# Performance work log

Measured on AMD Instinct MI355X. Metric: run time of the kernel, lower is better.

## Reference

```python
import jax, jax.numpy as jnp
import numpy as np

HEADS = 12
HEAD_SIZE = 64
NEG_BIG = 1e12


def _rope_sin_cos(seq_len, head_size, dtype):
    # embeddings[n, 2i] = sin(n * 10000^(-2i/d)), [n, 2i+1] = cos(...)
    pos = jnp.arange(seq_len, dtype=dtype)                      # [s]
    idx = jnp.arange(head_size // 2, dtype=dtype)               # [d/2]
    inv_freq = jnp.power(jnp.asarray(10000.0, dtype), -2.0 * idx / head_size)
    ang = jnp.einsum('n,d->nd', pos, inv_freq)                  # [s, d/2]
    # cos_pos / sin_pos: repeat_interleave each frequency twice -> [1, s, 1, d]
    cos = jnp.repeat(jnp.cos(ang), 2, axis=-1)[None, :, None, :]
    sin = jnp.repeat(jnp.sin(ang), 2, axis=-1)[None, :, None, :]
    return sin, cos


def _rotate_half_interleaved(x):
    # stack([-x[..., 1::2], x[..., ::2]], -1).reshape_as(x)
    x2 = jnp.stack([-x[..., 1::2], x[..., ::2]], axis=-1)
    return x2.reshape(x.shape)


def setup_inputs() -> dict:
    key = jax.random.key(0)
    k1, k2 = jax.random.split(key)
    bs, s, h = 16, 512, 768
    hidden = jax.random.normal(k1, (bs, s, h), dtype=jnp.float32)
    attention_mask = jnp.ones((bs, s), dtype=jnp.int32)
    W = jax.random.normal(k2, (h, HEADS * 2 * HEAD_SIZE), dtype=jnp.float32) * (h ** -0.5)
    b = jnp.zeros((HEADS * 2 * HEAD_SIZE,), dtype=jnp.float32)
    return {"hidden": hidden, "attention_mask": attention_mask, "W": W, "b": b}


def reference(hidden, attention_mask, W, b):
    bs, s, _ = hidden.shape
    x = hidden @ W + b                                           # [b, s, heads*2*hd]
    x = x.reshape(bs, s, HEADS, 2, HEAD_SIZE)
    qw, kw = x[..., 0, :], x[..., 1, :]                          # [b, s, h, d]

    sin, cos = _rope_sin_cos(s, HEAD_SIZE, hidden.dtype)
    qw = qw * cos + _rotate_half_interleaved(qw) * sin
    kw = kw * cos + _rotate_half_interleaved(kw) * sin

    logits = jnp.einsum('bmhd,bnhd->bhmn', qw, kw)               # [b, h, s, s]

    am = attention_mask.astype(logits.dtype)
    pad_mask = 1.0 - am[:, None, None, :] * am[:, None, :, None]
    logits = logits - pad_mask * NEG_BIG

    tril = jnp.tril(jnp.ones((s, s), dtype=logits.dtype), k=-1)  # strictly lower
    logits = logits - tril[None, None, :, :] * NEG_BIG

    return logits / (HEAD_SIZE ** 0.5)
```

## Files before the change

kernel.cpp:

```cpp
#include <hip/hip_runtime.h>
#include <math.h>

#define HEADS 12
#define HSZ   64
#define SEQ   512
#define HID   768
#define NOUT  1536
#define NEGQ  1.25e11f

typedef _Float16 f16x8 __attribute__((ext_vector_type(8)));
typedef _Float16 f16x4 __attribute__((ext_vector_type(4)));
typedef float    f32x4 __attribute__((ext_vector_type(4)));
typedef int      i32x4 __attribute__((ext_vector_type(4)));
typedef int      i32x8 __attribute__((ext_vector_type(8)));

__device__ __forceinline__ void async_ld16(const void* g, void* l) {
  __builtin_amdgcn_global_load_lds(
      (__attribute__((address_space(1))) void*)g,
      (__attribute__((address_space(3))) void*)l, 16, 0, 0);
}

__global__ __launch_bounds__(256) void prep_k(
    const float* __restrict__ hidden, const float* __restrict__ W,
    unsigned char* __restrict__ Xb8, unsigned char* __restrict__ Wt8,
    float2* __restrict__ tab)
{
  __shared__ float t_lds[32][33];
  const int b = blockIdx.x;
  const int t = threadIdx.x;
  if (b < 1152) {
    const int tk = b % 24, tn = b / 24;
    const int k0 = tk * 32, n0 = tn * 32;
    const int tx = t & 31, ty = t >> 5;
#pragma unroll
    for (int r = 0; r < 4; ++r)
      t_lds[ty + r * 8][tx] = W[(size_t)(k0 + ty + r * 8) * NOUT + n0 + tx];
    __syncthreads();
    const int nl = t >> 3, kg = t & 7;
    int w = __builtin_amdgcn_cvt_pk_fp8_f32(t_lds[kg * 4 + 0][nl],
                                            t_lds[kg * 4 + 1][nl], 0, false);
    w = __builtin_amdgcn_cvt_pk_fp8_f32(t_lds[kg * 4 + 2][nl],
                                        t_lds[kg * 4 + 3][nl], w, true);
    *(int*)&Wt8[(size_t)(n0 + nl) * HID + k0 + kg * 4] = w;
  } else if (b < 1152 + 1536) {
    const int base = (b - 1152) * 1024;
    const float4* src4 = (const float4*)hidden;
    int* dst = (int*)Xb8;
#pragma unroll
    for (int p = 0; p < 4; ++p) {
      const int i = base + p * 256 + t;
      const float4 v = src4[i];
      int o = __builtin_amdgcn_cvt_pk_fp8_f32(v.x, v.y, 0, false);
      o = __builtin_amdgcn_cvt_pk_fp8_f32(v.z, v.w, o, true);
      dst[i] = o;
    }
  } else {
    const int e = (b - 2688) * 256 + t;
    const int si = e >> 5, fi = e & 31;
    float inv = powf(10000.f, -(float)fi / 32.f);
    float ang = (float)si * inv;
    float sv, cv;
    sincosf(ang, &sv, &cv);
    tab[e] = make_float2(cv, sv);
  }
}

__global__ __launch_bounds__(256) void gemm1_k(
    const unsigned char* __restrict__ Xb8, const unsigned char* __restrict__ Wt8,
    const float* __restrict__ bias, const float2* __restrict__ tab,
    _Float16* __restrict__ qb, _Float16* __restrict__ kb)
{
  __shared__ __align__(16) int As4[4096];
  __shared__ __align__(16) int Bs4[4096];
  const int tid = threadIdx.x;
  const int lane = tid & 63;
  const int m0 = blockIdx.x * 128;
  const int n0 = blockIdx.y * 128;
  const int wm = ((tid >> 6) & 1) * 64;
  const int wn = (tid >> 7) * 64;
  const int lrow = lane & 15;
  const int q = lane >> 4;

  f32x4 acc[4][4] = {};

  for (int kt = 0; kt < 6; ++kt) {
    const int kbase = kt * 128;
#pragma unroll
    for (int c = 0; c < 4; ++c) {
      const int s = tid + c * 256;
      const int row = s >> 3, cc = s & 7;
      const int so = (((cc >> 1) ^ (row & 3)) << 5) + ((cc & 1) << 4);
      async_ld16(Xb8 + (size_t)(m0 + row) * HID + kbase + so, (char*)As4 + s * 16);
      async_ld16(Wt8 + (size_t)(n0 + row) * HID + kbase + so, (char*)Bs4 + s * 16);
    }
    __syncthreads();
    i32x8 af[4], bf[4];
#pragma unroll
    for (int i = 0; i < 4; ++i) {
      const int ra = wm + i * 16 + lrow;
      const int oa = ra * 32 + ((q ^ (ra & 3)) << 3);
      i32x4 lo = *(const i32x4*)&As4[oa];
      i32x4 hi = *(const i32x4*)&As4[oa + 4];
      af[i] = (i32x8){lo.x, lo.y, lo.z, lo.w, hi.x, hi.y, hi.z, hi.w};
      const int rb = wn + i * 16 + lrow;
      const int ob = rb * 32 + ((q ^ (rb & 3)) << 3);
      lo = *(const i32x4*)&Bs4[ob];
      hi = *(const i32x4*)&Bs4[ob + 4];
      bf[i] = (i32x8){lo.x, lo.y, lo.z, lo.w, hi.x, hi.y, hi.z, hi.w};
    }
#pragma unroll
    for (int i = 0; i < 4; ++i)
#pragma unroll
      for (int j = 0; j < 4; ++j)
        acc[i][j] = __builtin_amdgcn_mfma_scale_f32_16x16x128_f8f6f4(
            bf[j], af[i], acc[i][j], 0, 0,
            0, 0x7F7F7F7F, 0, 0x7F7F7F7F);
    __syncthreads();
  }

  {
    const int qlane = lane >> 4;
    const int rbase = wm + (lane & 15);
    f16x4* sdst = wn ? (f16x4*)Bs4 : (f16x4*)As4;
#pragma unroll
    for (int j = 0; j < 4; ++j) {
      const int d0 = j * 16 + qlane * 4;
      const int nb = n0 + wn + d0;
      const float4 b4 = *(const float4*)&bias[nb];
      const int fi0 = d0 >> 1;
#pragma unroll
      for (int i = 0; i < 4; ++i) {
        const int r = rbase + i * 16;
        const int m = m0 + r;
        const int si = m & (SEQ - 1);
        const float4 cs = *(const float4*)&tab[si * 32 + fi0];
        const float v0 = acc[i][j][0] + b4.x;
        const float v1 = acc[i][j][1] + b4.y;
        const float v2 = acc[i][j][2] + b4.z;
        const float v3 = acc[i][j][3] + b4.w;
        f16x4 o;
        o.x = (_Float16)fmaf(v0, cs.x, -v1 * cs.y);
        o.y = (_Float16)fmaf(v1, cs.x, v0 * cs.y);
        o.z = (_Float16)fmaf(v2, cs.z, -v3 * cs.w);
        o.w = (_Float16)fmaf(v3, cs.z, v2 * cs.w);
        sdst[r * 16 + ((d0 >> 2) ^ ((r & 7) << 1))] = o;
      }
    }
  }
  __syncthreads();

  {
    const int bb = m0 >> 9;
    const int si0 = m0 & (SEQ - 1);
    const int h = blockIdx.y;
    _Float16* qdst = qb + ((size_t)(bb * HEADS + h) * SEQ + si0) * HSZ;
    _Float16* kdst = kb + ((size_t)(bb * HEADS + h) * SEQ + si0) * HSZ;
#pragma unroll
    for (int p = 0; p < 4; ++p) {
      const int idx = p * 256 + tid;
      const int row = idx >> 3, v = idx & 7;
      const int sv = v ^ (row & 7);
      f16x8 qv = ((const f16x8*)As4)[row * 8 + sv];
      f16x8 kv = ((const f16x8*)Bs4)[row * 8 + sv];
      *(f16x8*)(qdst + row * HSZ + v * 8) = qv;
      *(f16x8*)(kdst + row * HSZ + v * 8) = kv;
    }
  }
}

__global__ __launch_bounds__(256) void gemm2_k(
    const _Float16* __restrict__ qb, const _Float16* __restrict__ kb,
    const int* __restrict__ am, float* __restrict__ out)
{
  __shared__ __align__(16) float sbuf[64 * 128];
  const int tid = threadIdx.x;
  const int bh = blockIdx.y;
  const int bb = bh / HEADS;
  const int mt = blockIdx.x >> 2, nt = blockIdx.x & 3;
  const int m0 = mt * 128, n0 = nt * 128;
  const int* amb = am + bb * SEQ;
  float* obase = out + (size_t)bh * SEQ * SEQ;

  if (nt < mt) {
#pragma unroll
    for (int p = 0; p < 16; ++p) {
      const int f = p * 256 + tid;
      const int row = f >> 5, c4 = (f & 31) * 4;
      const int m = m0 + row;
      const float amm = (float)amb[m];
      const int nb = n0 + c4;
      const int4 a4 = *(const int4*)&amb[nb];
      f32x4 v;
      v[0] = -(2.f - amm * (float)a4.x) * NEGQ;
      v[1] = -(2.f - amm * (float)a4.y) * NEGQ;
      v[2] = -(2.f - amm * (float)a4.z) * NEGQ;
      v[3] = -(2.f - amm * (float)a4.w) * NEGQ;
      __builtin_nontemporal_store(v, (f32x4*)&obase[(size_t)m * SEQ + nb]);
    }
    return;
  }

  const _Float16* qg = qb + (size_t)bh * SEQ * HSZ;
  const _Float16* kg = kb + (size_t)bh * SEQ * HSZ;
  const int lane = tid & 63;
  const int wm = ((tid >> 6) & 1) * 64;
  const int wn = (tid >> 7) * 64;
  const int lrow = lane & 15;
  const int lk = (lane >> 4) * 8;

  f16x8 af[4][2], bf[4][2];
#pragma unroll
  for (int i = 0; i < 4; ++i)
#pragma unroll
    for (int h = 0; h < 2; ++h) {
      af[i][h] = *(const f16x8*)(qg + (size_t)(m0 + wm + i * 16 + lrow) * HSZ + h * 32 + lk);
      bf[i][h] = *(const f16x8*)(kg + (size_t)(n0 + wn + i * 16 + lrow) * HSZ + h * 32 + lk);
    }

  f32x4 acc[4][4] = {};
#pragma unroll
  for (int h = 0; h < 2; ++h)
#pragma unroll
    for (int i = 0; i < 4; ++i)
#pragma unroll
      for (int j = 0; j < 4; ++j)
        acc[i][j] = __builtin_amdgcn_mfma_f32_16x16x32_f16(bf[j][h], af[i][h], acc[i][j], 0, 0, 0);

  const int qlane = lane >> 4;
  const int rloc = lane & 15;
  const int wmp = wm >> 6;
  for (int ph = 0; ph < 2; ++ph) {
    if (wmp == ph) {
#pragma unroll
      for (int i = 0; i < 4; ++i) {
        const int r = i * 16 + rloc;
        const int m = m0 + wm + r;
        const float amm = (float)amb[m];
#pragma unroll
        for (int j = 0; j < 4; ++j) {
          const int nb = n0 + wn + j * 16 + qlane * 4;
          const int4 a4 = *(const int4*)&amb[nb];
          f32x4 v;
          v[0] = fmaf(acc[i][j][0], 0.125f,
                      -((float)(nb + 0 < m) + (1.f - amm * (float)a4.x)) * NEGQ);
          v[1] = fmaf(acc[i][j][1], 0.125f,
                      -((float)(nb + 1 < m) + (1.f - amm * (float)a4.y)) * NEGQ);
          v[2] = fmaf(acc[i][j][2], 0.125f,
                      -((float)(nb + 2 < m) + (1.f - amm * (float)a4.z)) * NEGQ);
          v[3] = fmaf(acc[i][j][3], 0.125f,
                      -((float)(nb + 3 < m) + (1.f - amm * (float)a4.w)) * NEGQ);
          const int t = ((wn >> 2) + j * 4 + qlane) ^ (r & 7);
          *(f32x4*)&sbuf[r * 128 + t * 4] = v;
        }
      }
    }
    __syncthreads();
    const int rowbase = m0 + ph * 64;
#pragma unroll
    for (int p = 0; p < 8; ++p) {
      const int idx = p * 256 + tid;
      const int row = idx >> 5, t = idx & 31;
      f32x4 v = *(const f32x4*)&sbuf[row * 128 + ((t ^ (row & 7)) * 4)];
      __builtin_nontemporal_store(
          v, (f32x4*)&obase[(size_t)(rowbase + row) * SEQ + n0 + t * 4]);
    }
    __syncthreads();
  }
}

extern "C" void kernel_launch(void* const* d_in, const int* in_sizes, int n_in,
                              void* d_out, int out_size, void* d_ws, size_t ws_size,
                              hipStream_t stream) {
  const float* hidden = (const float*)d_in[0];
  const int*   am     = (const int*)d_in[1];
  const float* W      = (const float*)d_in[2];
  const float* bias   = (const float*)d_in[3];
  float* out = (float*)d_out;
  char* ws = (char*)d_ws;
  unsigned char* Xb8 = (unsigned char*)(ws);
  unsigned char* Wt8 = (unsigned char*)(ws + 6291456);
  _Float16* qb = (_Float16*)(ws + 7471104);
  _Float16* kb = (_Float16*)(ws + 20054016);
  float2*   tab = (float2*)(ws + 32636928);

  prep_k<<<dim3(2752), dim3(256), 0, stream>>>(hidden, W, Xb8, Wt8, tab);
  gemm1_k<<<dim3(64, 12), dim3(256), 0, stream>>>(Xb8, Wt8, bias, tab, qb, kb);
  gemm2_k<<<dim3(16, 192), dim3(256), 0, stream>>>(qb, kb, am, out);
}
```

Baseline: 266.3 us.

## Fuse prep, projection GEMM and logits GEMM into one persistent kernel with grid barriers

Merges the three launches into a single persistent kernel. Blocks loop over virtual block indices for each phase, and phases are separated by software grid barriers built on atomic counters. The counters live in the first words of the output buffer and are zeroed by a memset before launch. The aim is to remove inter-kernel launch gaps and drains. In exchange the grid is capped at occupancy times CU count, and the barriers spin. The counter words are later overwritten with logits while slower blocks may still be polling them, which risks a hang or early release.

New measurement: 387.4 us. 1.45x slower.

```diff
diff --git a/kernel.cpp b/kernel.cpp
--- a/kernel.cpp
+++ b/kernel.cpp
@@ -20,251 +20,267 @@
       (__attribute__((address_space(3))) void*)l, 16, 0, 0);
 }
 
-__global__ __launch_bounds__(256) void prep_k(
-    const float* __restrict__ hidden, const float* __restrict__ W,
+union SMem {
+  struct { int As4[4096]; int Bs4[4096]; } g1;
+  float sbuf[64 * 128];
+  float t_lds[32][33];
+};
+
+__device__ __forceinline__ void grid_barrier(unsigned* cnt, unsigned target) {
+  __syncthreads();
+  if (threadIdx.x == 0) {
+    __hip_atomic_fetch_add(cnt, 1u, __ATOMIC_RELEASE, __HIP_MEMORY_SCOPE_AGENT);
+    while (__hip_atomic_load(cnt, __ATOMIC_ACQUIRE, __HIP_MEMORY_SCOPE_AGENT) < target)
+      __builtin_amdgcn_s_sleep(8);
+  }
+  __syncthreads();
+}
+
+__global__ __launch_bounds__(256, 3) void fused_k(
+    const float* __restrict__ hidden, const int* __restrict__ am,
+    const float* __restrict__ W, const float* __restrict__ bias,
+    float* __restrict__ out,
     unsigned char* __restrict__ Xb8, unsigned char* __restrict__ Wt8,
+    _Float16* __restrict__ qb, _Float16* __restrict__ kb,
     float2* __restrict__ tab)
 {
-  __shared__ float t_lds[32][33];
-  const int b = blockIdx.x;
+  __shared__ __align__(16) SMem sm;
   const int t = threadIdx.x;
-  if (b < 1152) {
-    const int tk = b % 24, tn = b / 24;
-    const int k0 = tk * 32, n0 = tn * 32;
-    const int tx = t & 31, ty = t >> 5;
-#pragma unroll
-    for (int r = 0; r < 4; ++r)
-      t_lds[ty + r * 8][tx] = W[(size_t)(k0 + ty + r * 8) * NOUT + n0 + tx];
+  const int nblk = gridDim.x;
+
+  for (int vb = blockIdx.x; vb < 2752; vb += nblk) {
+    if (vb < 1152) {
+      const int tk = vb % 24, tn = vb / 24;
+      const int k0 = tk * 32, n0 = tn * 32;
+      const int tx = t & 31, ty = t >> 5;
+#pragma unroll
+      for (int r = 0; r < 4; ++r)
+        sm.t_lds[ty + r * 8][tx] = W[(size_t)(k0 + ty + r * 8) * NOUT + n0 + tx];
+      __syncthreads();
+      const int nl = t >> 3, kg = t & 7;
+      int w = __builtin_amdgcn_cvt_pk_fp8_f32(sm.t_lds[kg * 4 + 0][nl],
+                                              sm.t_lds[kg * 4 + 1][nl], 0, false);
+      w = __builtin_amdgcn_cvt_pk_fp8_f32(sm.t_lds[kg * 4 + 2][nl],
+                                          sm.t_lds[kg * 4 + 3][nl], w, true);
+      *(int*)&Wt8[(size_t)(n0 + nl) * HID + k0 + kg * 4] = w;
+      __syncthreads();
+    } else if (vb < 2688) {
+      const int base = (vb - 1152) * 1024;
+      const float4* src4 = (const float4*)hidden;
+      int* dst = (int*)Xb8;
+#pragma unroll
+      for (int p = 0; p < 4; ++p) {
+        const int i = base + p * 256 + t;
+        const float4 v = src4[i];
+        int o = __builtin_amdgcn_cvt_pk_fp8_f32(v.x, v.y, 0, false);
+        o = __builtin_amdgcn_cvt_pk_fp8_f32(v.z, v.w, o, true);
+        dst[i] = o;
+      }
+    } else {
+      const int e = (vb - 2688) * 256 + t;
+      const int si = e >> 5, fi = e & 31;
+      float inv = powf(10000.f, -(float)fi / 32.f);
+      float ang = (float)si * inv;
+      float sv, cv;
+      sincosf(ang, &sv, &cv);
+      tab[e] = make_float2(cv, sv);
+    }
+  }
+  grid_barrier((unsigned*)out, nblk);
+
+  for (int vb = blockIdx.x; vb < 768; vb += nblk) {
+    const int tid = t;
+    const int lane = tid & 63;
+    const int m0 = (vb & 63) * 128;
+    const int hH = vb >> 6;
+    const int n0 = hH * 128;
+    const int wm = ((tid >> 6) & 1) * 64;
+    const int wn = (tid >> 7) * 64;
+    const int lrow = lane & 15;
+    const int q = lane >> 4;
+
+    f32x4 acc[4][4] = {};
+
+    for (int kt = 0; kt < 6; ++kt) {
+      const int kbase = kt * 128;
+#pragma unroll
+      for (int c = 0; c < 4; ++c) {
+        const int s = tid + c * 256;
+        const int row = s >> 3, cc = s & 7;
+        const int so = (((cc >> 1) ^ (row & 3)) << 5) + ((cc & 1) << 4);
+        async_ld16(Xb8 + (size_t)(m0 + row) * HID + kbase + so, (char*)sm.g1.As4 + s * 16);
+        async_ld16(Wt8 + (size_t)(n0 + row) * HID + kbase + so, (char*)sm.g1.Bs4 + s * 16);
+      }
+      __syncthreads();
+      i32x8 af[4], bf[4];
+#pragma unroll
+      for (int i = 0; i < 4; ++i) {
+        const int ra = wm + i * 16 + lrow;
+        const int oa = ra * 32 + ((q ^ (ra & 3)) << 3);
+        i32x4 lo = *(const i32x4*)&sm.g1.As4[oa];
+        i32x4 hi = *(const i32x4*)&sm.g1.As4[oa + 4];
+        af[i] = (i32x8){lo.x, lo.y, lo.z, lo.w, hi.x, hi.y, hi.z, hi.w};
+        const int rb = wn + i * 16 + lrow;
+        const int ob = rb * 32 + ((q ^ (rb & 3)) << 3);
+        lo = *(const i32x4*)&sm.g1.Bs4[ob];
+        hi = *(const i32x4*)&sm.g1.Bs4[ob + 4];
+        bf[i] = (i32x8){lo.x, lo.y, lo.z, lo.w, hi.x, hi.y, hi.z, hi.w};
+      }
+#pragma unroll
+      for (int i = 0; i < 4; ++i)
+#pragma unroll
+        for (int j = 0; j < 4; ++j)
+          acc[i][j] = __builtin_amdgcn_mfma_scale_f32_16x16x128_f8f6f4(
+              bf[j], af[i], acc[i][j], 0, 0,
+              0, 0x7F7F7F7F, 0, 0x7F7F7F7F);
+      __syncthreads();
+    }
+
+    {
+      const int qlane = lane >> 4;
+      const int rbase = wm + (lane & 15);
+      f16x4* sdst = wn ? (f16x4*)sm.g1.Bs4 : (f16x4*)sm.g1.As4;
+#pragma unroll
+      for (int j = 0; j < 4; ++j) {
+        const int d0 = j * 16 + qlane * 4;
+        const int nb = n0 + wn + d0;
+        const float4 b4 = *(const float4*)&bias[nb];
+        const int fi0 = d0 >> 1;
+#pragma unroll
+        for (int i = 0; i < 4; ++i) {
+          const int r = rbase + i * 16;
+          const int m = m0 + r;
+          const int si = m & (SEQ - 1);
+          const float4 cs = *(const float4*)&tab[si * 32 + fi0];
+          const float v0 = acc[i][j][0] + b4.x;
+          const float v1 = acc[i][j][1] + b4.y;
+          const float v2 = acc[i][j][2] + b4.z;
+          const float v3 = acc[i][j][3] + b4.w;
+          f16x4 o;
+          o.x = (_Float16)fmaf(v0, cs.x, -v1 * cs.y);
+          o.y = (_Float16)fmaf(v1, cs.x, v0 * cs.y);
+          o.z = (_Float16)fmaf(v2, cs.z, -v3 * cs.w);
+          o.w = (_Float16)fmaf(v3, cs.z, v2 * cs.w);
+          sdst[r * 16 + ((d0 >> 2) ^ ((r & 7) << 1))] = o;
+        }
+      }
+    }
     __syncthreads();
-    const int nl = t >> 3, kg = t & 7;
-    int w = __builtin_amdgcn_cvt_pk_fp8_f32(t_lds[kg * 4 + 0][nl],
-                                            t_lds[kg * 4 + 1][nl], 0, false);
-    w = __builtin_amdgcn_cvt_pk_fp8_f32(t_lds[kg * 4 + 2][nl],
-                                        t_lds[kg * 4 + 3][nl], w, true);
-    *(int*)&Wt8[(size_t)(n0 + nl) * HID + k0 + kg * 4] = w;
-  } else if (b < 1152 + 1536) {
-    const int base = (b - 1152) * 1024;
-    const float4* src4 = (const float4*)hidden;
-    int* dst = (int*)Xb8;
-#pragma unroll
-    for (int p = 0; p < 4; ++p) {
-      const int i = base + p * 256 + t;
-      const float4 v = src4[i];
-      int o = __builtin_amdgcn_cvt_pk_fp8_f32(v.x, v.y, 0, false);
-      o = __builtin_amdgcn_cvt_pk_fp8_f32(v.z, v.w, o, true);
-      dst[i] = o;
-    }
-  } else {
-    const int e = (b - 2688) * 256 + t;
-    const int si = e >> 5, fi = e & 31;
-    float inv = powf(10000.f, -(float)fi / 32.f);
-    float ang = (float)si * inv;
-    float sv, cv;
-    sincosf(ang, &sv, &cv);
-    tab[e] = make_float2(cv, sv);
-  }
-}
-
-__global__ __launch_bounds__(256) void gemm1_k(
-    const unsigned char* __restrict__ Xb8, const unsigned char* __restrict__ Wt8,
-    const float* __restrict__ bias, const float2* __restrict__ tab,
-    _Float16* __restrict__ qb, _Float16* __restrict__ kb)
-{
-  __shared__ __align__(16) int As4[4096];
-  __shared__ __align__(16) int Bs4[4096];
-  const int tid = threadIdx.x;
-  const int lane = tid & 63;
-  const int m0 = blockIdx.x * 128;
-  const int n0 = blockIdx.y * 128;
-  const int wm = ((tid >> 6) & 1) * 64;
-  const int wn = (tid >> 7) * 64;
-  const int lrow = lane & 15;
-  const int q = lane >> 4;
-
-  f32x4 acc[4][4] = {};
-
-  for (int kt = 0; kt < 6; ++kt) {
-    const int kbase = kt * 128;
-#pragma unroll
-    for (int c = 0; c < 4; ++c) {
-      const int s = tid + c * 256;
-      const int row = s >> 3, cc = s & 7;
-      const int so = (((cc >> 1) ^ (row & 3)) << 5) + ((cc & 1) << 4);
-      async_ld16(Xb8 + (size_t)(m0 + row) * HID + kbase + so, (char*)As4 + s * 16);
-      async_ld16(Wt8 + (size_t)(n0 + row) * HID + kbase + so, (char*)Bs4 + s * 16);
-    }
-    __syncthreads();
-    i32x8 af[4], bf[4];
-#pragma unroll
-    for (int i = 0; i < 4; ++i) {
-      const int ra = wm + i * 16 + lrow;
-      const int oa = ra * 32 + ((q ^ (ra & 3)) << 3);
-      i32x4 lo = *(const i32x4*)&As4[oa];
-      i32x4 hi = *(const i32x4*)&As4[oa + 4];
-      af[i] = (i32x8){lo.x, lo.y, lo.z, lo.w, hi.x, hi.y, hi.z, hi.w};
-      const int rb = wn + i * 16 + lrow;
-      const int ob = rb * 32 + ((q ^ (rb & 3)) << 3);
-      lo = *(const i32x4*)&Bs4[ob];
-      hi = *(const i32x4*)&Bs4[ob + 4];
-      bf[i] = (i32x8){lo.x, lo.y, lo.z, lo.w, hi.x, hi.y, hi.z, hi.w};
-    }
-#pragma unroll
-    for (int i = 0; i < 4; ++i)
-#pragma unroll
-      for (int j = 0; j < 4; ++j)
-        acc[i][j] = __builtin_amdgcn_mfma_scale_f32_16x16x128_f8f6f4(
-            bf[j], af[i], acc[i][j], 0, 0,
-            0, 0x7F7F7F7F, 0, 0x7F7F7F7F);
+
+    {
+      const int bb = m0 >> 9;
+      const int si0 = m0 & (SEQ - 1);
+      _Float16* qdst = qb + ((size_t)(bb * HEADS + hH) * SEQ + si0) * HSZ;
+      _Float16* kdst = kb + ((size_t)(bb * HEADS + hH) * SEQ + si0) * HSZ;
+#pragma unroll
+      for (int p = 0; p < 4; ++p) {
+        const int idx = p * 256 + tid;
+        const int row = idx >> 3, v = idx & 7;
+        const int sv = v ^ (row & 7);
+        f16x8 qv = ((const f16x8*)sm.g1.As4)[row * 8 + sv];
+        f16x8 kv = ((const f16x8*)sm.g1.Bs4)[row * 8 + sv];
+        *(f16x8*)(qdst + row * HSZ + v * 8) = qv;
+        *(f16x8*)(kdst + row * HSZ + v * 8) = kv;
+      }
+    }
     __syncthreads();
   }
-
-  {
+  grid_barrier((unsigned*)out + 1, nblk);
+
+  for (int vb = blockIdx.x; vb < 3072; vb += nblk) {
+    const int tid = t;
+    const int bh = vb >> 4;
+    const int bb = bh / HEADS;
+    const int mt = (vb & 15) >> 2, nt = vb & 3;
+    const int m0 = mt * 128, n0 = nt * 128;
+    const int* amb = am + bb * SEQ;
+    float* obase = out + (size_t)bh * SEQ * SEQ;
+
+    if (nt < mt) {
+#pragma unroll
+      for (int p = 0; p < 16; ++p) {
+        const int f = p * 256 + tid;
+        const int row = f >> 5, c4 = (f & 31) * 4;
+        const int m = m0 + row;
+        const float amm = (float)amb[m];
+        const int nb = n0 + c4;
+        const int4 a4 = *(const int4*)&amb[nb];
+        f32x4 v;
+        v[0] = -(2.f - amm * (float)a4.x) * NEGQ;
+        v[1] = -(2.f - amm * (float)a4.y) * NEGQ;
+        v[2] = -(2.f - amm * (float)a4.z) * NEGQ;
+        v[3] = -(2.f - amm * (float)a4.w) * NEGQ;
+        __builtin_nontemporal_store(v, (f32x4*)&obase[(size_t)m * SEQ + nb]);
+      }
+      continue;
+    }
+
+    const _Float16* qg = qb + (size_t)bh * SEQ * HSZ;
+    const _Float16* kg = kb + (size_t)bh * SEQ * HSZ;
+    const int lane = tid & 63;
+    const int wm = ((tid >> 6) & 1) * 64;
+    const int wn = (tid >> 7) * 64;
+    const int lrow = lane & 15;
+    const int lk = (lane >> 4) * 8;
+
+    f16x8 af[4][2], bf[4][2];
+#pragma unroll
+    for (int i = 0; i < 4; ++i)
+#pragma unroll
+      for (int h = 0; h < 2; ++h) {
+        af[i][h] = *(const f16x8*)(qg + (size_t)(m0 + wm + i * 16 + lrow) * HSZ + h * 32 + lk);
+        bf[i][h] = *(const f16x8*)(kg + (size_t)(n0 + wn + i * 16 + lrow) * HSZ + h * 32 + lk);
+      }
+
+    f32x4 acc[4][4] = {};
+#pragma unroll
+    for (int h = 0; h < 2; ++h)
+#pragma unroll
+      for (int i = 0; i < 4; ++i)
+#pragma unroll
+        for (int j = 0; j < 4; ++j)
+          acc[i][j] = __builtin_amdgcn_mfma_f32_16x16x32_f16(bf[j][h], af[i][h], acc[i][j], 0, 0, 0);
+
     const int qlane = lane >> 4;
-    const int rbase = wm + (lane & 15);
-    f16x4* sdst = wn ? (f16x4*)Bs4 : (f16x4*)As4;
-#pragma unroll
-    for (int j = 0; j < 4; ++j) {
-      const int d0 = j * 16 + qlane * 4;
-      const int nb = n0 + wn + d0;
-      const float4 b4 = *(const float4*)&bias[nb];
-      const int fi0 = d0 >> 1;
-#pragma unroll
-      for (int i = 0; i < 4; ++i) {
-        const int r = rbase + i * 16;
-        const int m = m0 + r;
-        const int si = m & (SEQ - 1);
-        const float4 cs = *(const float4*)&tab[si * 32 + fi0];
-        const float v0 = acc[i][j][0] + b4.x;
-        const float v1 = acc[i][j][1] + b4.y;
-        const float v2 = acc[i][j][2] + b4.z;
-        const float v3 = acc[i][j][3] + b4.w;
-        f16x4 o;
-        o.x = (_Float16)fmaf(v0, cs.x, -v1 * cs.y);
-        o.y = (_Float16)fmaf(v1, cs.x, v0 * cs.y);
-        o.z = (_Float16)fmaf(v2, cs.z, -v3 * cs.w);
-        o.w = (_Float16)fmaf(v3, cs.z, v2 * cs.w);
-        sdst[r * 16 + ((d0 >> 2) ^ ((r & 7) << 1))] = o;
-      }
-    }
-  }
-  __syncthreads();
-
-  {
-    const int bb = m0 >> 9;
-    const int si0 = m0 & (SEQ - 1);
-    const int h = blockIdx.y;
-    _Float16* qdst = qb + ((size_t)(bb * HEADS + h) * SEQ + si0) * HSZ;
-    _Float16* kdst = kb + ((size_t)(bb * HEADS + h) * SEQ + si0) * HSZ;
-#pragma unroll
-    for (int p = 0; p < 4; ++p) {
-      const int idx = p * 256 + tid;
-      const int row = idx >> 3, v = idx & 7;
-      const int sv = v ^ (row & 7);
-      f16x8 qv = ((const f16x8*)As4)[row * 8 + sv];
-      f16x8 kv = ((const f16x8*)Bs4)[row * 8 + sv];
-      *(f16x8*)(qdst + row * HSZ + v * 8) = qv;
-      *(f16x8*)(kdst + row * HSZ + v * 8) = kv;
-    }
-  }
-}
-
-__global__ __launch_bounds__(256) void gemm2_k(
-    const _Float16* __restrict__ qb, const _Float16* __restrict__ kb,
-    const int* __restrict__ am, float* __restrict__ out)
-{
-  __shared__ __align__(16) float sbuf[64 * 128];
-  const int tid = threadIdx.x;
-  const int bh = blockIdx.y;
-  const int bb = bh / HEADS;
-  const int mt = blockIdx.x >> 2, nt = blockIdx.x & 3;
-  const int m0 = mt * 128, n0 = nt * 128;
-  const int* amb = am + bb * SEQ;
-  float* obase = out + (size_t)bh * SEQ * SEQ;
-
-  if (nt < mt) {
-#pragma unroll
-    for (int p = 0; p < 16; ++p) {
-      const int f = p * 256 + tid;
-      const int row = f >> 5, c4 = (f & 31) * 4;
-      const int m = m0 + row;
-      const float amm = (float)amb[m];
-      const int nb = n0 + c4;
-      const int4 a4 = *(const int4*)&amb[nb];
-      f32x4 v;
-      v[0] = -(2.f - amm * (float)a4.x) * NEGQ;
-      v[1] = -(2.f - amm * (float)a4.y) * NEGQ;
-      v[2] = -(2.f - amm * (float)a4.z) * NEGQ;
-      v[3] = -(2.f - amm * (float)a4.w) * NEGQ;
-      __builtin_nontemporal_store(v, (f32x4*)&obase[(size_t)m * SEQ + nb]);
-    }
-    return;
-  }
-
-  const _Float16* qg = qb + (size_t)bh * SEQ * HSZ;
-  const _Float16* kg = kb + (size_t)bh * SEQ * HSZ;
-  const int lane = tid & 63;
-  const int wm = ((tid >> 6) & 1) * 64;
-  const int wn = (tid >> 7) * 64;
-  const int lrow = lane & 15;
-  const int lk = (lane >> 4) * 8;
-
-  f16x8 af[4][2], bf[4][2];
-#pragma unroll
-  for (int i = 0; i < 4; ++i)
-#pragma unroll
-    for (int h = 0; h < 2; ++h) {
-      af[i][h] = *(const f16x8*)(qg + (size_t)(m0 + wm + i * 16 + lrow) * HSZ + h * 32 + lk);
-      bf[i][h] = *(const f16x8*)(kg + (size_t)(n0 + wn + i * 16 + lrow) * HSZ + h * 32 + lk);
-    }
-
-  f32x4 acc[4][4] = {};
-#pragma unroll
-  for (int h = 0; h < 2; ++h)
-#pragma unroll
-    for (int i = 0; i < 4; ++i)
-#pragma unroll
-      for (int j = 0; j < 4; ++j)
-        acc[i][j] = __builtin_amdgcn_mfma_f32_16x16x32_f16(bf[j][h], af[i][h], acc[i][j], 0, 0, 0);
-
-  const int qlane = lane >> 4;
-  const int rloc = lane & 15;
-  const int wmp = wm >> 6;
-  for (int ph = 0; ph < 2; ++ph) {
-    if (wmp == ph) {
-#pragma unroll
-      for (int i = 0; i < 4; ++i) {
-        const int r = i * 16 + rloc;
-        const int m = m0 + wm + r;
-        const float amm = (float)amb[m];
-#pragma unroll
-        for (int j = 0; j < 4; ++j) {
-          const int nb = n0 + wn + j * 16 + qlane * 4;
-          const int4 a4 = *(const int4*)&amb[nb];
-          f32x4 v;
-          v[0] = fmaf(acc[i][j][0], 0.125f,
-                      -((float)(nb + 0 < m) + (1.f - amm * (float)a4.x)) * NEGQ);
-          v[1] = fmaf(acc[i][j][1], 0.125f,
-                      -((float)(nb + 1 < m) + (1.f - amm * (float)a4.y)) * NEGQ);
-          v[2] = fmaf(acc[i][j][2], 0.125f,
-                      -((float)(nb + 2 < m) + (1.f - amm * (float)a4.z)) * NEGQ);
-          v[3] = fmaf(acc[i][j][3], 0.125f,
-                      -((float)(nb + 3 < m) + (1.f - amm * (float)a4.w)) * NEGQ);
-          const int t = ((wn >> 2) + j * 4 + qlane) ^ (r & 7);
-          *(f32x4*)&sbuf[r * 128 + t * 4] = v;
+    const int rloc = lane & 15;
+    const int wmp = wm >> 6;
+    for (int ph = 0; ph < 2; ++ph) {
+      if (wmp == ph) {
+#pragma unroll
+        for (int i = 0; i < 4; ++i) {
+          const int r = i * 16 + rloc;
+          const int m = m0 + wm + r;
+          const float amm = (float)amb[m];
+#pragma unroll
+          for (int j = 0; j < 4; ++j) {
+            const int nb = n0 + wn + j * 16 + qlane * 4;
+            const int4 a4 = *(const int4*)&amb[nb];
+            f32x4 v;
+            v[0] = fmaf(acc[i][j][0], 0.125f,
+                        -((float)(nb + 0 < m) + (1.f - amm * (float)a4.x)) * NEGQ);
+            v[1] = fmaf(acc[i][j][1], 0.125f,
+                        -((float)(nb + 1 < m) + (1.f - amm * (float)a4.y)) * NEGQ);
+            v[2] = fmaf(acc[i][j][2], 0.125f,
+                        -((float)(nb + 2 < m) + (1.f - amm * (float)a4.z)) * NEGQ);
+            v[3] = fmaf(acc[i][j][3], 0.125f,
+                        -((float)(nb + 3 < m) + (1.f - amm * (float)a4.w)) * NEGQ);
+            const int tt = ((wn >> 2) + j * 4 + qlane) ^ (r & 7);
+            *(f32x4*)&sm.sbuf[r * 128 + tt * 4] = v;
+          }
         }
       }
-    }
-    __syncthreads();
-    const int rowbase = m0 + ph * 64;
-#pragma unroll
-    for (int p = 0; p < 8; ++p) {
-      const int idx = p * 256 + tid;
-      const int row = idx >> 5, t = idx & 31;
-      f32x4 v = *(const f32x4*)&sbuf[row * 128 + ((t ^ (row & 7)) * 4)];
-      __builtin_nontemporal_store(
-          v, (f32x4*)&obase[(size_t)(rowbase + row) * SEQ + n0 + t * 4]);
-    }
-    __syncthreads();
+      __syncthreads();
+      const int rowbase = m0 + ph * 64;
+#pragma unroll
+      for (int p = 0; p < 8; ++p) {
+        const int idx = p * 256 + tid;
+        const int row = idx >> 5, tt = idx & 31;
+        f32x4 v = *(const f32x4*)&sm.sbuf[row * 128 + ((tt ^ (row & 7)) * 4)];
+        __builtin_nontemporal_store(
+            v, (f32x4*)&obase[(size_t)(rowbase + row) * SEQ + n0 + tt * 4]);
+      }
+      __syncthreads();
+    }
   }
 }
 
@@ -283,7 +299,16 @@
   _Float16* kb = (_Float16*)(ws + 20054016);
   float2*   tab = (float2*)(ws + 32636928);
 
-  prep_k<<<dim3(2752), dim3(256), 0, stream>>>(hidden, W, Xb8, Wt8, tab);
-  gemm1_k<<<dim3(64, 12), dim3(256), 0, stream>>>(Xb8, Wt8, bias, tab, qb, kb);
-  gemm2_k<<<dim3(16, 192), dim3(256), 0, stream>>>(qb, kb, am, out);
+  int dev = 0, cus = 256, nb = 0;
+  hipGetDevice(&dev);
+  hipDeviceGetAttribute(&cus, hipDeviceAttributeMultiprocessorCount, dev);
+  hipOccupancyMaxActiveBlocksPerMultiprocessor(&nb, fused_k, 256, 0);
+  if (nb < 1) nb = 1;
+  if (cus < 1) cus = 256;
+  long cap = (long)nb * cus;
+  int grid = (int)(cap < 768 ? cap : 768);
+
+  hipMemsetAsync(d_out, 0, 8, stream);
+  fused_k<<<dim3(grid), dim3(256), 0, stream>>>(hidden, am, W, bias, out,
+                                                Xb8, Wt8, qb, kb, tab);
 }
```
